# Kernel tuning notes

Hardware: AMD Instinct MI355X
Metric: run time of the kernel (lower is better)

## Reference

```python
import jax, jax.numpy as jnp
import numpy as np

N, E = 50000, 800000
IN_DIM, HID, HEADS, OUT = 128, 16, 8, 64
SLOPE = 0.2  # DGL GATConv default negative_slope


def setup_inputs() -> dict:
    key = jax.random.key(0)
    ks = jax.random.split(key, 12)
    return {
        "features": jax.random.normal(ks[0], (N, IN_DIM), jnp.float32),
        "src": jax.random.randint(ks[1], (E,), 0, N, jnp.int32),
        "dst": jax.random.randint(ks[2], (E,), 0, N, jnp.int32),
        "w": jax.random.uniform(ks[3], (E,), jnp.float32),
        "W1": jax.random.normal(ks[4], (IN_DIM, HEADS * HID), jnp.float32) / np.sqrt(IN_DIM),
        "al1": jax.random.normal(ks[5], (HEADS, HID), jnp.float32) * 0.1,
        "ar1": jax.random.normal(ks[6], (HEADS, HID), jnp.float32) * 0.1,
        "b1": jnp.zeros((HEADS * HID,), jnp.float32),
        "W2": jax.random.normal(ks[7], (HEADS * HID, OUT), jnp.float32) / np.sqrt(HEADS * HID),
        "al2": jax.random.normal(ks[8], (1, OUT), jnp.float32) * 0.1,
        "ar2": jax.random.normal(ks[9], (1, OUT), jnp.float32) * 0.1,
        "b2": jnp.zeros((OUT,), jnp.float32),
    }


def _gat_layer(x, src, dst, w, W, al, ar, b, heads, dout, act):
    """DGL GATConv with edge_weight: proj -> edge attn -> edge softmax(dst) -> * w -> scatter-sum."""
    n = x.shape[0]
    h = (x @ W).reshape(n, heads, dout)                 # [N,H,D]
    el = (h * al[None]).sum(-1)                         # [N,H] left attn logits
    er = (h * ar[None]).sum(-1)                         # [N,H] right attn logits
    e = el[src] + er[dst]                               # [E,H]
    e = jnp.where(e > 0, e, SLOPE * e)                  # leaky_relu
    m = jax.ops.segment_max(e, dst, num_segments=n)     # per-dst max for stable softmax
    a = jnp.exp(e - m[dst])
    z = jax.ops.segment_sum(a, dst, num_segments=n)
    a = (a / z[dst]) * w[:, None]                       # edge softmax scaled by edge weight
    msg = a[:, :, None] * h[src]                        # [E,H,D] gathered weighted messages
    rst = jax.ops.segment_sum(msg, dst, num_segments=n) # [N,H,D] scatter aggregation
    rst = rst + b.reshape(1, heads, dout)               # GATConv bias
    return act(rst) if act is not None else rst


def reference(features, src, dst, w, W1, al1, ar1, b1, W2, al2, ar2, b2):
    h = _gat_layer(features, src, dst, w, W1, al1, ar1, b1, HEADS, HID, jax.nn.relu)
    h = jax.nn.relu(h).reshape(N, HEADS * HID)          # outer F.relu + flatten(1)
    out = _gat_layer(h, src, dst, w, W2, al2, ar2, b2, 1, OUT, None)
    return out.squeeze(1)                               # [N,OUT]
```

## Files before the change

kernel.cpp:

```cpp
#include <hip/hip_runtime.h>
#include <hip/hip_fp16.h>

#define NN 50000
#define NE 800000

#define NBK 196
#define BSH 8
#define BMASK 255
#define SCAP 5120
#define CHUNK 2048
#define NBLK_A ((NE + CHUNK - 1) / CHUNK)
#define NBLK_P ((NN + 63) / 64)
#define GPAD 4

typedef _Float16 f16x8 __attribute__((ext_vector_type(8)));
typedef float f32x4 __attribute__((ext_vector_type(4)));

__device__ __forceinline__ float h2f_hi(unsigned int u) {
    return __half2float(__ushort_as_half((unsigned short)(u >> 16)));
}

__global__ __launch_bounds__(256) void init_k(const float* __restrict__ W1,
                                              const float* __restrict__ W2,
                                              const float* __restrict__ al1,
                                              const float* __restrict__ ar1,
                                              const float* __restrict__ al2,
                                              const float* __restrict__ ar2,
                                              __half* __restrict__ w1t,
                                              __half* __restrict__ w2t,
                                              int* __restrict__ gcur) {
    const int i = blockIdx.x * 256 + threadIdx.x;
    {
        const int k = i >> 7, n = i & 127;
        w1t[n * 128 + k] = __float2half(W1[i]);
    }
    if (i < 128 * 64) {
        const int k = i >> 6, n = i & 63;
        w2t[n * 128 + k] = __float2half(W2[i]);
    }
    if (i < 2048) {
        const int j = i >> 7, k = i & 127;
        const int h = j & 7;
        const float* ap = (j < 8) ? al1 : ar1;
        float s = 0.f;
        #pragma unroll
        for (int d = 0; d < 16; d++)
            s += W1[k * 128 + h * 16 + d] * ap[h * 16 + d];
        w1t[(size_t)(128 + j) * 128 + k] = __float2half(s);
    }
    if (i < 256) {
        const int j = i >> 7, k = i & 127;
        const float* ap = (j == 0) ? al2 : ar2;
        float s = 0.f;
        #pragma unroll
        for (int d = 0; d < 64; d++)
            s += W2[k * 64 + d] * ap[d];
        w2t[(size_t)(64 + j) * 128 + k] = __float2half(s);
    }
    if (i < 14 * 128) {
        w2t[(size_t)(66 + (i >> 7)) * 128 + (i & 127)] = __float2half(0.f);
    }
    if (i < NBK) gcur[i << GPAD] = 0;
}

__global__ __launch_bounds__(256) void sortA_proj1_k(const int* __restrict__ src,
                                                     const int* __restrict__ dst,
                                                     const float* __restrict__ wE,
                                                     int* __restrict__ gcur,
                                                     int2* __restrict__ stage,
                                                     const float* __restrict__ x,
                                                     const __half* __restrict__ w1t,
                                                     __half* __restrict__ h1h,
                                                     float* __restrict__ el1,
                                                     float* __restrict__ er1) {
    const int t = threadIdx.x;
    if (blockIdx.x < NBLK_A) {
        __shared__ int hcnt[NBK], lexcl[NBK], lcur[NBK], gbase[NBK];
        __shared__ int wsum[4];
        __shared__ int2 lbuf[CHUNK];
        const int e0 = blockIdx.x * CHUNK;
        const int ne = min(CHUNK, NE - e0);
        if (t < NBK) { hcnt[t] = 0; lcur[t] = 0; }
        __syncthreads();
        for (int i = t; i < ne; i += 256) atomicAdd(&hcnt[dst[e0 + i] >> BSH], 1);
        __syncthreads();
        {
            const int lane = t & 63, wid = t >> 6;
            const int v = (t < NBK) ? hcnt[t] : 0;
            int s = v;
            #pragma unroll
            for (int off = 1; off < 64; off <<= 1) {
                int u = __shfl_up(s, off, 64);
                if (lane >= off) s += u;
            }
            if (lane == 63) wsum[wid] = s;
            __syncthreads();
            int add = 0;
            for (int w = 0; w < wid; w++) add += wsum[w];
            if (t < NBK) lexcl[t] = s - v + add;
        }
        __syncthreads();
        if (t < NBK && hcnt[t] > 0) gbase[t] = atomicAdd(&gcur[t << GPAD], hcnt[t]);
        __syncthreads();
        for (int i = t; i < ne; i += 256) {
            const int d = dst[e0 + i];
            const int b = d >> BSH;
            const int r = atomicAdd(&lcur[b], 1);
            lbuf[lexcl[b] + r] = make_int2((src[e0 + i] & 0xFFFF) | ((d & BMASK) << 16) | (b << 24),
                                           __float_as_int(wE[e0 + i]));
        }
        __syncthreads();
        for (int i = t; i < ne; i += 256) {
            const int2 v = lbuf[i];
            const int b = (unsigned int)v.x >> 24;
            const int pos = gbase[b] + (i - lexcl[b]);
            stage[(size_t)b * SCAP + pos] = v;
        }
    } else {
        const int bid = blockIdx.x - NBLK_A;
        const int l = t & 63, wv = t >> 6;
        const int rbase = bid * 64 + wv * 16;
        const int cl = l & 15, kg = l >> 4;
        const int arow = rbase + cl;
        const float* xrow = x + (size_t)(arow < NN ? arow : NN - 1) * 128;
        f16x8 afrag[4];
        #pragma unroll
        for (int ks = 0; ks < 4; ks++) {
            const float4 u0 = *(const float4*)(xrow + ks * 32 + kg * 8);
            const float4 u1 = *(const float4*)(xrow + ks * 32 + kg * 8 + 4);
            f16x8 a;
            a[0] = (_Float16)u0.x; a[1] = (_Float16)u0.y; a[2] = (_Float16)u0.z; a[3] = (_Float16)u0.w;
            a[4] = (_Float16)u1.x; a[5] = (_Float16)u1.y; a[6] = (_Float16)u1.z; a[7] = (_Float16)u1.w;
            afrag[ks] = a;
        }
        f32x4 acc[9];
        #pragma unroll
        for (int nt = 0; nt < 9; nt++) { acc[nt][0]=0.f; acc[nt][1]=0.f; acc[nt][2]=0.f; acc[nt][3]=0.f; }
        #pragma unroll
        for (int nt = 0; nt < 9; nt++) {
            const f16x8* bp = (const f16x8*)(w1t + (size_t)(nt * 16 + cl) * 128 + kg * 8);
            #pragma unroll
            for (int ks = 0; ks < 4; ks++)
                acc[nt] = __builtin_amdgcn_mfma_f32_16x16x32_f16(afrag[ks], bp[ks * 4], acc[nt], 0, 0, 0);
        }
        const int orow0 = rbase + kg * 4;
        #pragma unroll
        for (int nt = 0; nt < 8; nt++) {
            const int col = nt * 16 + cl;
            #pragma unroll
            for (int r = 0; r < 4; r++) {
                const int orow = orow0 + r;
                if (orow < NN) h1h[(size_t)orow * 128 + col] = __float2half(acc[nt][r]);
            }
        }
        #pragma unroll
        for (int r = 0; r < 4; r++) {
            const int orow = orow0 + r;
            if (orow < NN) {
                if (cl < 8) el1[(size_t)orow * 8 + cl] = acc[8][r];
                else        er1[(size_t)orow * 8 + (cl - 8)] = acc[8][r];
            }
        }
    }
}

__global__ __launch_bounds__(1024) void sortB_k(const int* __restrict__ gcur,
                                                const int2* __restrict__ stage,
                                                int* __restrict__ offs,
                                                unsigned int* __restrict__ csr) {
    __shared__ int cnt[256], cur[256], gall[NBK];
    __shared__ int wsum[4];
    __shared__ int sbase;
    const int b = blockIdx.x, t = threadIdx.x;
    if (t < NBK) gall[t] = gcur[t << GPAD];
    if (t < 256) cnt[t] = 0;
    __syncthreads();
    const int nb = gall[b];
    if (t < 64) {
        int part = 0;
        for (int i = t; i < b; i += 64) part += gall[i];
        #pragma unroll
        for (int m = 1; m < 64; m <<= 1) part += __shfl_xor(part, m, 64);
        if (t == 0) sbase = part;
    }
    const int2* sp = stage + (size_t)b * SCAP;
    for (int i = t; i < nb; i += 1024) atomicAdd(&cnt[(sp[i].x >> 16) & BMASK], 1);
    __syncthreads();
    const int base = sbase;
    const int dlo = b << BSH;
    {
        const int lane = t & 63, wid = t >> 6;
        const int v = (t < 256) ? cnt[t] : 0;
        int s = v;
        #pragma unroll
        for (int off = 1; off < 64; off <<= 1) {
            int u = __shfl_up(s, off, 64);
            if (lane >= off) s += u;
        }
        if (t < 256 && lane == 63) wsum[wid] = s;
        __syncthreads();
        if (t < 256) {
            int add = 0;
            for (int w = 0; w < wid; w++) add += wsum[w];
            const int excl = s - v + add;
            cur[t] = excl;
            if (dlo + t < NN) offs[dlo + t] = base + excl;
        }
        if (b == NBK - 1 && t == 0) offs[NN] = base + nb;
    }
    __syncthreads();
    for (int i = t; i < nb; i += 1024) {
        const int2 pr = sp[i];
        const int dloc = (pr.x >> 16) & BMASK;
        const int sv = pr.x & 0xFFFF;
        const int r = atomicAdd(&cur[dloc], 1);
        const __half hw = __float2half(__int_as_float(pr.y));
        csr[base + r] = (unsigned int)sv | ((unsigned int)__half_as_ushort(hw) << 16);
    }
}

__global__ __launch_bounds__(128) void agg1_k(const int* __restrict__ offs,
                                              const unsigned int* __restrict__ csr,
                                              const __half* __restrict__ h1h,
                                              const float* __restrict__ el1,
                                              const float* __restrict__ er1,
                                              const float* __restrict__ b1,
                                              __half* __restrict__ h2in_h) {
    const int t = threadIdx.x, w = t >> 6, l = t & 63;
    const int nA = blockIdx.x * 4 + w * 2;
    const int nB = nA + 1;
    const int begA = offs[nA], degA = offs[nA + 1] - begA;
    const int begB = offs[nB], degB = offs[nB + 1] - begB;
    const int h = l & 7, e0 = l >> 3, e1 = e0 + 8;
    const int g = l & 15, es = l >> 4, hg = g >> 1;
    const float erA = er1[(size_t)nA * 8 + h];
    const float erB = er1[(size_t)nB * 8 + h];
    float zA = 0.f, zB = 0.f;
    float accA[8], accB[8];
    #pragma unroll
    for (int j = 0; j < 8; j++) { accA[j] = 0.f; accB[j] = 0.f; }
    const float4* hp4 = (const float4*)h1h;
    const int dmax = max(degA, degB);

    for (int base = 0; base < dmax; base += 16) {
        int pr = 0;
        if (l < 16) { if (base + l < degA) pr = (int)csr[begA + base + l]; }
        else if (l < 32) { const int e = l - 16; if (base + e < degB) pr = (int)csr[begB + base + e]; }
        const unsigned int pA0 = (unsigned int)__shfl(pr, e0, 64);
        const unsigned int pA1 = (unsigned int)__shfl(pr, e1, 64);
        const unsigned int pB0 = (unsigned int)__shfl(pr, 16 + e0, 64);
        const unsigned int pB1 = (unsigned int)__shfl(pr, 16 + e1, 64);
        float lgA0 = -1e30f, lgA1 = -1e30f, lgB0 = -1e30f, lgB1 = -1e30f;
        if (base + e0 < degA) { const float v = el1[(size_t)(pA0 & 0xFFFF) * 8 + h] + erA; lgA0 = v > 0.f ? v : 0.2f * v; }
        if (base + e1 < degA) { const float v = el1[(size_t)(pA1 & 0xFFFF) * 8 + h] + erA; lgA1 = v > 0.f ? v : 0.2f * v; }
        if (base + e0 < degB) { const float v = el1[(size_t)(pB0 & 0xFFFF) * 8 + h] + erB; lgB0 = v > 0.f ? v : 0.2f * v; }
        if (base + e1 < degB) { const float v = el1[(size_t)(pB1 & 0xFFFF) * 8 + h] + erB; lgB1 = v > 0.f ? v : 0.2f * v; }
        const float eA0 = __expf(lgA0), eA1 = __expf(lgA1);
        const float eB0 = __expf(lgB0), eB1 = __expf(lgB1);
        zA += eA0 + eA1;
        zB += eB0 + eB1;
        const float pwA0 = eA0 * h2f_hi(pA0), pwA1 = eA1 * h2f_hi(pA1);
        const float pwB0 = eB0 * h2f_hi(pB0), pwB1 = eB1 * h2f_hi(pB1);
        const int sA0 = __shfl(pr, es, 64) & 0xFFFF;
        const int sA1 = __shfl(pr, es + 4, 64) & 0xFFFF;
        const int sA2 = __shfl(pr, es + 8, 64) & 0xFFFF;
        const int sA3 = __shfl(pr, es + 12, 64) & 0xFFFF;
        const int sB0 = __shfl(pr, 16 + es, 64) & 0xFFFF;
        const int sB1 = __shfl(pr, 16 + es + 4, 64) & 0xFFFF;
        const int sB2 = __shfl(pr, 16 + es + 8, 64) & 0xFFFF;
        const int sB3 = __shfl(pr, 16 + es + 12, 64) & 0xFFFF;
        const float qA0 = __shfl(pwA0, es * 8 + hg, 64);
        const float qA1 = __shfl(pwA0, (es + 4) * 8 + hg, 64);
        const float qA2 = __shfl(pwA1, es * 8 + hg, 64);
        const float qA3 = __shfl(pwA1, (es + 4) * 8 + hg, 64);
        const float qB0 = __shfl(pwB0, es * 8 + hg, 64);
        const float qB1 = __shfl(pwB0, (es + 4) * 8 + hg, 64);
        const float qB2 = __shfl(pwB1, es * 8 + hg, 64);
        const float qB3 = __shfl(pwB1, (es + 4) * 8 + hg, 64);
        const float4 vA0 = hp4[(size_t)sA0 * 16 + g];
        const float4 vA1 = hp4[(size_t)sA1 * 16 + g];
        const float4 vA2 = hp4[(size_t)sA2 * 16 + g];
        const float4 vA3 = hp4[(size_t)sA3 * 16 + g];
        const float4 vB0 = hp4[(size_t)sB0 * 16 + g];
        const float4 vB1 = hp4[(size_t)sB1 * 16 + g];
        const float4 vB2 = hp4[(size_t)sB2 * 16 + g];
        const float4 vB3 = hp4[(size_t)sB3 * 16 + g];
        #pragma unroll
        for (int q = 0; q < 4; q++) {
            const float2 fA0 = __half22float2(((const __half2*)&vA0)[q]);
            const float2 fA1 = __half22float2(((const __half2*)&vA1)[q]);
            const float2 fA2 = __half22float2(((const __half2*)&vA2)[q]);
            const float2 fA3 = __half22float2(((const __half2*)&vA3)[q]);
            accA[2 * q]     = fmaf(qA0, fA0.x, fmaf(qA1, fA1.x, fmaf(qA2, fA2.x, fmaf(qA3, fA3.x, accA[2 * q]))));
            accA[2 * q + 1] = fmaf(qA0, fA0.y, fmaf(qA1, fA1.y, fmaf(qA2, fA2.y, fmaf(qA3, fA3.y, accA[2 * q + 1]))));
            const float2 fB0 = __half22float2(((const __half2*)&vB0)[q]);
            const float2 fB1 = __half22float2(((const __half2*)&vB1)[q]);
            const float2 fB2 = __half22float2(((const __half2*)&vB2)[q]);
            const float2 fB3 = __half22float2(((const __half2*)&vB3)[q]);
            accB[2 * q]     = fmaf(qB0, fB0.x, fmaf(qB1, fB1.x, fmaf(qB2, fB2.x, fmaf(qB3, fB3.x, accB[2 * q]))));
            accB[2 * q + 1] = fmaf(qB0, fB0.y, fmaf(qB1, fB1.y, fmaf(qB2, fB2.y, fmaf(qB3, fB3.y, accB[2 * q + 1]))));
        }
    }
    zA += __shfl_xor(zA, 8, 64);  zA += __shfl_xor(zA, 16, 64);  zA += __shfl_xor(zA, 32, 64);
    zB += __shfl_xor(zB, 8, 64);  zB += __shfl_xor(zB, 16, 64);  zB += __shfl_xor(zB, 32, 64);
    #pragma unroll
    for (int j = 0; j < 8; j++) {
        accA[j] += __shfl_xor(accA[j], 16, 64);
        accA[j] += __shfl_xor(accA[j], 32, 64);
        accB[j] += __shfl_xor(accB[j], 16, 64);
        accB[j] += __shfl_xor(accB[j], 32, 64);
    }
    const float zgA = __shfl(zA, hg, 64);
    const float zgB = __shfl(zB, hg, 64);
    const float4* b4 = (const float4*)b1;
    const float4 bb0 = b4[g * 2], bb1 = b4[g * 2 + 1];
    if (l < 32) {
        const bool isA = (l < 16);
        const int n = isA ? nA : nB;
        const int deg = isA ? degA : degB;
        const float zg = isA ? zgA : zgB;
        const float inv = (deg > 0) ? 1.f / zg : 0.f;
        float ac[8];
        #pragma unroll
        for (int j = 0; j < 8; j++) ac[j] = isA ? accA[j] : accB[j];
        __half hv[8];
        hv[0] = __float2half(fmaxf(ac[0] * inv + bb0.x, 0.f));
        hv[1] = __float2half(fmaxf(ac[1] * inv + bb0.y, 0.f));
        hv[2] = __float2half(fmaxf(ac[2] * inv + bb0.z, 0.f));
        hv[3] = __float2half(fmaxf(ac[3] * inv + bb0.w, 0.f));
        hv[4] = __float2half(fmaxf(ac[4] * inv + bb1.x, 0.f));
        hv[5] = __float2half(fmaxf(ac[5] * inv + bb1.y, 0.f));
        hv[6] = __float2half(fmaxf(ac[6] * inv + bb1.z, 0.f));
        hv[7] = __float2half(fmaxf(ac[7] * inv + bb1.w, 0.f));
        *(int4*)(h2in_h + (size_t)n * 128 + g * 8) = *(const int4*)hv;
    }
}

__global__ __launch_bounds__(256) void proj2_k(const __half* __restrict__ xh,
                                               const __half* __restrict__ w2t,
                                               __half* __restrict__ h2h,
                                               float* __restrict__ el2,
                                               float* __restrict__ er2) {
    const int t = threadIdx.x, l = t & 63, wv = t >> 6;
    const int rbase = blockIdx.x * 64 + wv * 16;
    const int cl = l & 15, kg = l >> 4;
    const int arow = rbase + cl;
    const __half* xrow = xh + (size_t)(arow < NN ? arow : NN - 1) * 128;
    f16x8 afrag[4];
    #pragma unroll
    for (int ks = 0; ks < 4; ks++)
        afrag[ks] = *(const f16x8*)(xrow + ks * 32 + kg * 8);
    f32x4 acc[5];
    #pragma unroll
    for (int nt = 0; nt < 5; nt++) { acc[nt][0]=0.f; acc[nt][1]=0.f; acc[nt][2]=0.f; acc[nt][3]=0.f; }
    #pragma unroll
    for (int nt = 0; nt < 5; nt++) {
        const f16x8* bp = (const f16x8*)(w2t + (size_t)(nt * 16 + cl) * 128 + kg * 8);
        #pragma unroll
        for (int ks = 0; ks < 4; ks++)
            acc[nt] = __builtin_amdgcn_mfma_f32_16x16x32_f16(afrag[ks], bp[ks * 4], acc[nt], 0, 0, 0);
    }
    const int orow0 = rbase + kg * 4;
    #pragma unroll
    for (int nt = 0; nt < 4; nt++) {
        const int col = nt * 16 + cl;
        #pragma unroll
        for (int r = 0; r < 4; r++) {
            const int orow = orow0 + r;
            if (orow < NN) h2h[(size_t)orow * 64 + col] = __float2half(acc[nt][r]);
        }
    }
    #pragma unroll
    for (int r = 0; r < 4; r++) {
        const int orow = orow0 + r;
        if (orow < NN) {
            if (cl == 0) el2[orow] = acc[4][r];
            else if (cl == 1) er2[orow] = acc[4][r];
        }
    }
}

__global__ __launch_bounds__(128) void agg2_k(const int* __restrict__ offs,
                                              const unsigned int* __restrict__ csr,
                                              const __half* __restrict__ h2h,
                                              const float* __restrict__ el2,
                                              const float* __restrict__ er2,
                                              const float* __restrict__ b2,
                                              float* __restrict__ out) {
    const int t = threadIdx.x, w = t >> 6, l = t & 63;
    const int nA = blockIdx.x * 4 + w * 2;
    const int nB = nA + 1;
    const int begA = offs[nA], degA = offs[nA + 1] - begA;
    const int begB = offs[nB], degB = offs[nB + 1] - begB;
    const int g = l & 7, es = l >> 3;
    const float erdA = er2[nA], erdB = er2[nB];
    float zl = 0.f;
    float accA[8], accB[8];
    #pragma unroll
    for (int j = 0; j < 8; j++) { accA[j] = 0.f; accB[j] = 0.f; }
    const float4* hp4 = (const float4*)h2h;
    const int dmax = max(degA, degB);

    for (int base = 0; base < dmax; base += 16) {
        int pr = 0;
        bool okE = false;
        if (l < 16) { okE = (base + l < degA); if (okE) pr = (int)csr[begA + base + l]; }
        else if (l < 32) { const int e = l - 16; okE = (base + e < degB); if (okE) pr = (int)csr[begB + base + e]; }
        float pw = 0.f;
        if (okE) {
            const float er = (l < 16) ? erdA : erdB;
            const float v = el2[(unsigned int)pr & 0xFFFF] + er;
            const float lg = v > 0.f ? v : 0.2f * v;
            const float p = __expf(lg);
            zl += p;
            pw = p * h2f_hi((unsigned int)pr);
        }
        const int sA0 = __shfl(pr, es, 64) & 0xFFFF;
        const int sA1 = __shfl(pr, es + 8, 64) & 0xFFFF;
        const int sB0 = __shfl(pr, 16 + es, 64) & 0xFFFF;
        const int sB1 = __shfl(pr, 16 + es + 8, 64) & 0xFFFF;
        const float qA0 = __shfl(pw, es, 64);
        const float qA1 = __shfl(pw, es + 8, 64);
        const float qB0 = __shfl(pw, 16 + es, 64);
        const float qB1 = __shfl(pw, 16 + es + 8, 64);
        const float4 vA0 = hp4[(size_t)sA0 * 8 + g];
        const float4 vA1 = hp4[(size_t)sA1 * 8 + g];
        const float4 vB0 = hp4[(size_t)sB0 * 8 + g];
        const float4 vB1 = hp4[(size_t)sB1 * 8 + g];
        #pragma unroll
        for (int q = 0; q < 4; q++) {
            const float2 fA0 = __half22float2(((const __half2*)&vA0)[q]);
            const float2 fA1 = __half22float2(((const __half2*)&vA1)[q]);
            accA[2 * q]     = fmaf(qA0, fA0.x, fmaf(qA1, fA1.x, accA[2 * q]));
            accA[2 * q + 1] = fmaf(qA0, fA0.y, fmaf(qA1, fA1.y, accA[2 * q + 1]));
            const float2 fB0 = __half22float2(((const __half2*)&vB0)[q]);
            const float2 fB1 = __half22float2(((const __half2*)&vB1)[q]);
            accB[2 * q]     = fmaf(qB0, fB0.x, fmaf(qB1, fB1.x, accB[2 * q]));
            accB[2 * q + 1] = fmaf(qB0, fB0.y, fmaf(qB1, fB1.y, accB[2 * q + 1]));
        }
    }
    zl += __shfl_xor(zl, 1, 64);
    zl += __shfl_xor(zl, 2, 64);
    zl += __shfl_xor(zl, 4, 64);
    zl += __shfl_xor(zl, 8, 64);
    const float zA = __shfl(zl, 0, 64);
    const float zB = __shfl(zl, 16, 64);
    #pragma unroll
    for (int j = 0; j < 8; j++) {
        accA[j] += __shfl_xor(accA[j], 8, 64);
        accA[j] += __shfl_xor(accA[j], 16, 64);
        accA[j] += __shfl_xor(accA[j], 32, 64);
        accB[j] += __shfl_xor(accB[j], 8, 64);
        accB[j] += __shfl_xor(accB[j], 16, 64);
        accB[j] += __shfl_xor(accB[j], 32, 64);
    }
    const float4* b4 = (const float4*)b2;
    const float4 bb0 = b4[g * 2], bb1 = b4[g * 2 + 1];
    if (l < 8 || (l >= 16 && l < 24)) {
        const bool isA = (l < 8);
        const int n = isA ? nA : nB;
        const int deg = isA ? degA : degB;
        const float z = isA ? zA : zB;
        const float inv = (deg > 0) ? 1.f / z : 0.f;
        float ac[8];
        #pragma unroll
        for (int j = 0; j < 8; j++) ac[j] = isA ? accA[j] : accB[j];
        float4 o0, o1;
        o0.x = ac[0] * inv + bb0.x;
        o0.y = ac[1] * inv + bb0.y;
        o0.z = ac[2] * inv + bb0.z;
        o0.w = ac[3] * inv + bb0.w;
        o1.x = ac[4] * inv + bb1.x;
        o1.y = ac[5] * inv + bb1.y;
        o1.z = ac[6] * inv + bb1.z;
        o1.w = ac[7] * inv + bb1.w;
        float4* op = (float4*)(out + (size_t)n * 64 + g * 8);
        op[0] = o0; op[1] = o1;
    }
}


extern "C" void kernel_launch(void* const* d_in, const int* in_sizes, int n_in,
                              void* d_out, int out_size, void* d_ws, size_t ws_size,
                              hipStream_t stream) {
    const float* feat = (const float*)d_in[0];
    const int*   srcv = (const int*)d_in[1];
    const int*   dstv = (const int*)d_in[2];
    const float* wE   = (const float*)d_in[3];
    const float* W1   = (const float*)d_in[4];
    const float* al1  = (const float*)d_in[5];
    const float* ar1  = (const float*)d_in[6];
    const float* b1   = (const float*)d_in[7];
    const float* W2   = (const float*)d_in[8];
    const float* al2  = (const float*)d_in[9];
    const float* ar2  = (const float*)d_in[10];
    const float* b2   = (const float*)d_in[11];
    float* out = (float*)d_out;

    char* ws = (char*)d_ws;
    size_t off = 0;
    auto take = [&](size_t bytes) -> char* {
        char* pp = ws + off;
        off = (off + bytes + 255) & ~(size_t)255;
        return pp;
    };
    __half* h1h   = (__half*)take((size_t)NN * 128 * 2);
    __half* h2h   = (__half*)take((size_t)NN * 64 * 2);
    __half* h2in_h= (__half*)take((size_t)NN * 128 * 2);
    float* el1  = (float*)take((size_t)NN * 8 * 4);
    float* er1  = (float*)take((size_t)NN * 8 * 4);
    float* el2  = (float*)take((size_t)NN * 4);
    float* er2  = (float*)take((size_t)NN * 4);
    int* offs   = (int*)take((size_t)(NN + 1) * 4);
    unsigned int* csr = (unsigned int*)take((size_t)NE * 4);
    int* gcur   = (int*)take((size_t)(NBK << GPAD) * 4);
    __half* w1t = (__half*)take((size_t)144 * 128 * 2);
    __half* w2t = (__half*)take((size_t)80 * 128 * 2);
    int2* stage = (int2*)h2in_h;

    init_k<<<64, 256, 0, stream>>>(W1, W2, al1, ar1, al2, ar2, w1t, w2t, gcur);
    sortA_proj1_k<<<NBLK_A + NBLK_P, 256, 0, stream>>>(srcv, dstv, wE, gcur, stage,
                                                       feat, w1t, h1h, el1, er1);
    sortB_k<<<NBK, 1024, 0, stream>>>(gcur, stage, offs, csr);
    agg1_k<<<NN / 4, 128, 0, stream>>>(offs, csr, h1h, el1, er1, b1, h2in_h);
    proj2_k<<<(NN + 63) / 64, 256, 0, stream>>>(h2in_h, w2t, h2h, el2, er2);
    agg2_k<<<NN / 4, 128, 0, stream>>>(offs, csr, h2h, el2, er2, b2, out);
}
```

Measured before the change: 136.1 us.

## Partition layer-1 features by head pairs and split aggregation per head-pair slice

```diff
diff --git a/kernel.cpp b/kernel.cpp
--- a/kernel.cpp
+++ b/kernel.cpp
@@ -12,6 +12,7 @@
 #define NBLK_A ((NE + CHUNK - 1) / CHUNK)
 #define NBLK_P ((NN + 63) / 64)
 #define GPAD 4
+#define NB1 1563
 
 typedef _Float16 f16x8 __attribute__((ext_vector_type(8)));
 typedef float f32x4 __attribute__((ext_vector_type(4)));
@@ -70,7 +71,7 @@
                                                      int2* __restrict__ stage,
                                                      const float* __restrict__ x,
                                                      const __half* __restrict__ w1t,
-                                                     __half* __restrict__ h1h,
+                                                     __half* __restrict__ h1p,
                                                      float* __restrict__ el1,
                                                      float* __restrict__ er1) {
     const int t = threadIdx.x;
@@ -147,10 +148,12 @@
         #pragma unroll
         for (int nt = 0; nt < 8; nt++) {
             const int col = nt * 16 + cl;
+            const int hp = col >> 5, dd = col & 31;
             #pragma unroll
             for (int r = 0; r < 4; r++) {
                 const int orow = orow0 + r;
-                if (orow < NN) h1h[(size_t)orow * 128 + col] = __float2half(acc[nt][r]);
+                if (orow < NN)
+                    h1p[((size_t)hp * NN + orow) * 32 + dd] = __float2half(acc[nt][r]);
             }
         }
         #pragma unroll
@@ -219,120 +222,91 @@
     }
 }
 
-__global__ __launch_bounds__(128) void agg1_k(const int* __restrict__ offs,
+__global__ __launch_bounds__(256) void agg1_k(const int* __restrict__ offs,
                                               const unsigned int* __restrict__ csr,
-                                              const __half* __restrict__ h1h,
+                                              const __half* __restrict__ h1p,
                                               const float* __restrict__ el1,
                                               const float* __restrict__ er1,
                                               const float* __restrict__ b1,
                                               __half* __restrict__ h2in_h) {
-    const int t = threadIdx.x, w = t >> 6, l = t & 63;
-    const int nA = blockIdx.x * 4 + w * 2;
-    const int nB = nA + 1;
-    const int begA = offs[nA], degA = offs[nA + 1] - begA;
-    const int begB = offs[nB], degB = offs[nB + 1] - begB;
-    const int h = l & 7, e0 = l >> 3, e1 = e0 + 8;
-    const int g = l & 15, es = l >> 4, hg = g >> 1;
-    const float erA = er1[(size_t)nA * 8 + h];
-    const float erB = er1[(size_t)nB * 8 + h];
-    float zA = 0.f, zB = 0.f;
-    float accA[8], accB[8];
-    #pragma unroll
-    for (int j = 0; j < 8; j++) { accA[j] = 0.f; accB[j] = 0.f; }
-    const float4* hp4 = (const float4*)h1h;
-    const int dmax = max(degA, degB);
-
-    for (int base = 0; base < dmax; base += 16) {
-        int pr = 0;
-        if (l < 16) { if (base + l < degA) pr = (int)csr[begA + base + l]; }
-        else if (l < 32) { const int e = l - 16; if (base + e < degB) pr = (int)csr[begB + base + e]; }
-        const unsigned int pA0 = (unsigned int)__shfl(pr, e0, 64);
-        const unsigned int pA1 = (unsigned int)__shfl(pr, e1, 64);
-        const unsigned int pB0 = (unsigned int)__shfl(pr, 16 + e0, 64);
-        const unsigned int pB1 = (unsigned int)__shfl(pr, 16 + e1, 64);
-        float lgA0 = -1e30f, lgA1 = -1e30f, lgB0 = -1e30f, lgB1 = -1e30f;
-        if (base + e0 < degA) { const float v = el1[(size_t)(pA0 & 0xFFFF) * 8 + h] + erA; lgA0 = v > 0.f ? v : 0.2f * v; }
-        if (base + e1 < degA) { const float v = el1[(size_t)(pA1 & 0xFFFF) * 8 + h] + erA; lgA1 = v > 0.f ? v : 0.2f * v; }
-        if (base + e0 < degB) { const float v = el1[(size_t)(pB0 & 0xFFFF) * 8 + h] + erB; lgB0 = v > 0.f ? v : 0.2f * v; }
-        if (base + e1 < degB) { const float v = el1[(size_t)(pB1 & 0xFFFF) * 8 + h] + erB; lgB1 = v > 0.f ? v : 0.2f * v; }
-        const float eA0 = __expf(lgA0), eA1 = __expf(lgA1);
-        const float eB0 = __expf(lgB0), eB1 = __expf(lgB1);
-        zA += eA0 + eA1;
-        zB += eB0 + eB1;
-        const float pwA0 = eA0 * h2f_hi(pA0), pwA1 = eA1 * h2f_hi(pA1);
-        const float pwB0 = eB0 * h2f_hi(pB0), pwB1 = eB1 * h2f_hi(pB1);
-        const int sA0 = __shfl(pr, es, 64) & 0xFFFF;
-        const int sA1 = __shfl(pr, es + 4, 64) & 0xFFFF;
-        const int sA2 = __shfl(pr, es + 8, 64) & 0xFFFF;
-        const int sA3 = __shfl(pr, es + 12, 64) & 0xFFFF;
-        const int sB0 = __shfl(pr, 16 + es, 64) & 0xFFFF;
-        const int sB1 = __shfl(pr, 16 + es + 4, 64) & 0xFFFF;
-        const int sB2 = __shfl(pr, 16 + es + 8, 64) & 0xFFFF;
-        const int sB3 = __shfl(pr, 16 + es + 12, 64) & 0xFFFF;
-        const float qA0 = __shfl(pwA0, es * 8 + hg, 64);
-        const float qA1 = __shfl(pwA0, (es + 4) * 8 + hg, 64);
-        const float qA2 = __shfl(pwA1, es * 8 + hg, 64);
-        const float qA3 = __shfl(pwA1, (es + 4) * 8 + hg, 64);
-        const float qB0 = __shfl(pwB0, es * 8 + hg, 64);
-        const float qB1 = __shfl(pwB0, (es + 4) * 8 + hg, 64);
-        const float qB2 = __shfl(pwB1, es * 8 + hg, 64);
-        const float qB3 = __shfl(pwB1, (es + 4) * 8 + hg, 64);
-        const float4 vA0 = hp4[(size_t)sA0 * 16 + g];
-        const float4 vA1 = hp4[(size_t)sA1 * 16 + g];
-        const float4 vA2 = hp4[(size_t)sA2 * 16 + g];
-        const float4 vA3 = hp4[(size_t)sA3 * 16 + g];
-        const float4 vB0 = hp4[(size_t)sB0 * 16 + g];
-        const float4 vB1 = hp4[(size_t)sB1 * 16 + g];
-        const float4 vB2 = hp4[(size_t)sB2 * 16 + g];
-        const float4 vB3 = hp4[(size_t)sB3 * 16 + g];
+    const int t = threadIdx.x, wv = t >> 6, l = t & 63;
+    const int hp = (blockIdx.x & 7) >> 1;
+    const int h0 = hp * 2;
+    const int nb = (blockIdx.x >> 3) * 2 + (blockIdx.x & 1);
+    const int n = nb * 16 + wv * 4 + (l >> 4);
+    const int e = l & 15;
+    const bool nok = (n < NN);
+    const int nc = nok ? n : 0;
+    const int beg = offs[nc];
+    const int deg = nok ? (offs[nc + 1] - beg) : 0;
+    const float2 erv = *(const float2*)(er1 + (size_t)nc * 8 + h0);
+    float z0 = 0.f, z1 = 0.f;
+    float acc[32];
+    #pragma unroll
+    for (int j = 0; j < 32; j++) acc[j] = 0.f;
+    const __half* slice = h1p + (size_t)hp * NN * 32;
+
+    int dm = deg;
+    dm = max(dm, __shfl_xor(dm, 16, 64));
+    dm = max(dm, __shfl_xor(dm, 32, 64));
+
+    for (int base = 0; base < dm; base += 16) {
+        const bool ok = (base + e < deg);
+        const unsigned int c = ok ? csr[beg + base + e] : 0u;
+        const int sv = (int)(c & 0xFFFF);
+        const float2 elv = *(const float2*)(el1 + (size_t)sv * 8 + h0);
+        float lg0 = elv.x + erv.x; lg0 = lg0 > 0.f ? lg0 : 0.2f * lg0;
+        float lg1 = elv.y + erv.y; lg1 = lg1 > 0.f ? lg1 : 0.2f * lg1;
+        const float p0 = ok ? __expf(lg0) : 0.f;
+        const float p1 = ok ? __expf(lg1) : 0.f;
+        z0 += p0; z1 += p1;
+        const float wf = h2f_hi(c);
+        const float pw0 = p0 * wf, pw1 = p1 * wf;
+        const float4* vp = (const float4*)(slice + (size_t)sv * 32);
+        const float4 v0 = vp[0], v1 = vp[1], v2 = vp[2], v3 = vp[3];
         #pragma unroll
         for (int q = 0; q < 4; q++) {
-            const float2 fA0 = __half22float2(((const __half2*)&vA0)[q]);
-            const float2 fA1 = __half22float2(((const __half2*)&vA1)[q]);
-            const float2 fA2 = __half22float2(((const __half2*)&vA2)[q]);
-            const float2 fA3 = __half22float2(((const __half2*)&vA3)[q]);
-            accA[2 * q]     = fmaf(qA0, fA0.x, fmaf(qA1, fA1.x, fmaf(qA2, fA2.x, fmaf(qA3, fA3.x, accA[2 * q]))));
-            accA[2 * q + 1] = fmaf(qA0, fA0.y, fmaf(qA1, fA1.y, fmaf(qA2, fA2.y, fmaf(qA3, fA3.y, accA[2 * q + 1]))));
-            const float2 fB0 = __half22float2(((const __half2*)&vB0)[q]);
-            const float2 fB1 = __half22float2(((const __half2*)&vB1)[q]);
-            const float2 fB2 = __half22float2(((const __half2*)&vB2)[q]);
-            const float2 fB3 = __half22float2(((const __half2*)&vB3)[q]);
-            accB[2 * q]     = fmaf(qB0, fB0.x, fmaf(qB1, fB1.x, fmaf(qB2, fB2.x, fmaf(qB3, fB3.x, accB[2 * q]))));
-            accB[2 * q + 1] = fmaf(qB0, fB0.y, fmaf(qB1, fB1.y, fmaf(qB2, fB2.y, fmaf(qB3, fB3.y, accB[2 * q + 1]))));
-        }
-    }
-    zA += __shfl_xor(zA, 8, 64);  zA += __shfl_xor(zA, 16, 64);  zA += __shfl_xor(zA, 32, 64);
-    zB += __shfl_xor(zB, 8, 64);  zB += __shfl_xor(zB, 16, 64);  zB += __shfl_xor(zB, 32, 64);
-    #pragma unroll
-    for (int j = 0; j < 8; j++) {
-        accA[j] += __shfl_xor(accA[j], 16, 64);
-        accA[j] += __shfl_xor(accA[j], 32, 64);
-        accB[j] += __shfl_xor(accB[j], 16, 64);
-        accB[j] += __shfl_xor(accB[j], 32, 64);
-    }
-    const float zgA = __shfl(zA, hg, 64);
-    const float zgB = __shfl(zB, hg, 64);
-    const float4* b4 = (const float4*)b1;
-    const float4 bb0 = b4[g * 2], bb1 = b4[g * 2 + 1];
-    if (l < 32) {
-        const bool isA = (l < 16);
-        const int n = isA ? nA : nB;
-        const int deg = isA ? degA : degB;
-        const float zg = isA ? zgA : zgB;
-        const float inv = (deg > 0) ? 1.f / zg : 0.f;
-        float ac[8];
-        #pragma unroll
-        for (int j = 0; j < 8; j++) ac[j] = isA ? accA[j] : accB[j];
-        __half hv[8];
-        hv[0] = __float2half(fmaxf(ac[0] * inv + bb0.x, 0.f));
-        hv[1] = __float2half(fmaxf(ac[1] * inv + bb0.y, 0.f));
-        hv[2] = __float2half(fmaxf(ac[2] * inv + bb0.z, 0.f));
-        hv[3] = __float2half(fmaxf(ac[3] * inv + bb0.w, 0.f));
-        hv[4] = __float2half(fmaxf(ac[4] * inv + bb1.x, 0.f));
-        hv[5] = __float2half(fmaxf(ac[5] * inv + bb1.y, 0.f));
-        hv[6] = __float2half(fmaxf(ac[6] * inv + bb1.z, 0.f));
-        hv[7] = __float2half(fmaxf(ac[7] * inv + bb1.w, 0.f));
-        *(int4*)(h2in_h + (size_t)n * 128 + g * 8) = *(const int4*)hv;
+            const float2 f0 = __half22float2(((const __half2*)&v0)[q]);
+            const float2 f1 = __half22float2(((const __half2*)&v1)[q]);
+            const float2 f2 = __half22float2(((const __half2*)&v2)[q]);
+            const float2 f3 = __half22float2(((const __half2*)&v3)[q]);
+            acc[2 * q]      = fmaf(pw0, f0.x, acc[2 * q]);
+            acc[2 * q + 1]  = fmaf(pw0, f0.y, acc[2 * q + 1]);
+            acc[8 + 2 * q]     = fmaf(pw0, f1.x, acc[8 + 2 * q]);
+            acc[8 + 2 * q + 1] = fmaf(pw0, f1.y, acc[8 + 2 * q + 1]);
+            acc[16 + 2 * q]     = fmaf(pw1, f2.x, acc[16 + 2 * q]);
+            acc[16 + 2 * q + 1] = fmaf(pw1, f2.y, acc[16 + 2 * q + 1]);
+            acc[24 + 2 * q]     = fmaf(pw1, f3.x, acc[24 + 2 * q]);
+            acc[24 + 2 * q + 1] = fmaf(pw1, f3.y, acc[24 + 2 * q + 1]);
+        }
+    }
+    #pragma unroll
+    for (int m = 1; m < 16; m <<= 1) {
+        z0 += __shfl_xor(z0, m, 64);
+        z1 += __shfl_xor(z1, m, 64);
+    }
+    #pragma unroll
+    for (int j = 0; j < 32; j++) {
+        #pragma unroll
+        for (int m = 1; m < 16; m <<= 1)
+            acc[j] += __shfl_xor(acc[j], m, 64);
+    }
+    if (nok) {
+        const float inv0 = (deg > 0) ? 1.f / z0 : 0.f;
+        const float inv1 = (deg > 0) ? 1.f / z1 : 0.f;
+        const int d = 2 * e;
+        const float invd = (d < 16) ? inv0 : inv1;
+        float va = 0.f, vb = 0.f;
+        #pragma unroll
+        for (int j = 0; j < 32; j++) {
+            va = (j == 0 ? 0.f : va);
+            if (j == d) va = acc[j];
+            if (j == d + 1) vb = acc[j];
+        }
+        va = fmaxf(va * invd + b1[hp * 32 + d], 0.f);
+        vb = fmaxf(vb * invd + b1[hp * 32 + d + 1], 0.f);
+        __half2 hv = __floats2half2_rn(va, vb);
+        *(__half2*)(h2in_h + (size_t)n * 128 + hp * 32 + d) = hv;
     }
 }
 
@@ -504,7 +478,7 @@
         off = (off + bytes + 255) & ~(size_t)255;
         return pp;
     };
-    __half* h1h   = (__half*)take((size_t)NN * 128 * 2);
+    __half* h1p   = (__half*)take((size_t)NN * 128 * 2);
     __half* h2h   = (__half*)take((size_t)NN * 64 * 2);
     __half* h2in_h= (__half*)take((size_t)NN * 128 * 2);
     float* el1  = (float*)take((size_t)NN * 8 * 4);
@@ -520,9 +494,9 @@
 
     init_k<<<64, 256, 0, stream>>>(W1, W2, al1, ar1, al2, ar2, w1t, w2t, gcur);
     sortA_proj1_k<<<NBLK_A + NBLK_P, 256, 0, stream>>>(srcv, dstv, wE, gcur, stage,
-                                                       feat, w1t, h1h, el1, er1);
+                                                       feat, w1t, h1p, el1, er1);
     sortB_k<<<NBK, 1024, 0, stream>>>(gcur, stage, offs, csr);
-    agg1_k<<<NN / 4, 128, 0, stream>>>(offs, csr, h1h, el1, er1, b1, h2in_h);
+    agg1_k<<<NB1 * 8, 256, 0, stream>>>(offs, csr, h1p, el1, er1, b1, h2in_h);
     proj2_k<<<(NN + 63) / 64, 256, 0, stream>>>(h2in_h, w2t, h2h, el2, er2);
     agg2_k<<<NN / 4, 128, 0, stream>>>(offs, csr, h2h, el2, er2, b2, out);
 }
```

New measurement: 177.5 us. +30.4%, slower.
